# Kernel tuning notes

Measured on AMD Instinct MI355X. Metric: run time of the kernel, lower is better.

Reference implementation:

```python
import jax, jax.numpy as jnp
import numpy as np

MAX_THRESHOLD = 0.25  # init kwarg
B, S, D, E = 8, 4096, 512, 8


def setup_inputs() -> dict:
    key = jax.random.key(0)
    ks = jax.random.split(key, 5)
    scale = 1.0 / np.sqrt(D)
    return {
        "inputs": jax.random.normal(ks[0], (B, S, D), dtype=jnp.float32),
        "W_gate": jax.random.normal(ks[1], (D, E), dtype=jnp.float32) * scale,
        "b_gate": jnp.zeros((E,), dtype=jnp.float32),
        "W_thr": jax.random.normal(ks[2], (D, 1), dtype=jnp.float32) * scale,
        "b_thr": jnp.zeros((1,), dtype=jnp.float32),
        "W_exp": jax.random.normal(ks[3], (E, D, D), dtype=jnp.float32) * scale,
        "b_exp": jnp.zeros((E, D), dtype=jnp.float32),
    }


def reference(inputs, W_gate, b_gate, W_thr, b_thr, W_exp, b_exp):
    d = inputs.shape[-1]
    x = inputs.reshape(-1, d)  # [T, D]
    # gating
    gate_logits = jax.nn.softmax(x @ W_gate + b_gate, axis=-1)          # [T, E]
    thresholds = jax.nn.sigmoid(x @ W_thr + b_thr) * MAX_THRESHOLD      # [T, 1]
    adapted = gate_logits - thresholds                                  # [T, E]
    selected = (adapted >= 0).astype(x.dtype)                           # [T, E]
    weights = adapted * selected                                        # [T, E]
    wsum = jnp.sum(weights, axis=-1, keepdims=True)
    wsum = jnp.where(wsum == 0, jnp.ones_like(wsum), wsum)
    weights = weights / wsum
    # dense-equivalent of gather->expert->scatter (weights are 0 where unselected)
    ex_out = jnp.einsum('td,edf->etf', x, W_exp) + b_exp[:, None, :]    # [E, T, D]
    results = jnp.einsum('etf,te->tf', ex_out, weights)                 # [T, D]
    return results.reshape(inputs.shape[:-1] + (results.shape[-1],))
```

## Files before the change

kernel.cpp:

```cpp
#include <hip/hip_runtime.h>


#define T_TOKENS 32768
#define DDIM 512
#define KDIM 4096

typedef __attribute__((ext_vector_type(8))) short short8;
typedef __attribute__((ext_vector_type(4))) float floatx4;
typedef __bf16 bf16x2 __attribute__((ext_vector_type(2)));

__device__ __forceinline__ unsigned short f2bf(float f) {
    unsigned int u = __float_as_uint(f);
    u += 0x7FFFu + ((u >> 16) & 1u);
    return (unsigned short)(u >> 16);
}

__device__ __forceinline__ unsigned int pk2(float a, float b) {
#if __has_builtin(__builtin_amdgcn_cvt_pk_bf16_f32)
    bf16x2 v = __builtin_amdgcn_cvt_pk_bf16_f32(a, b);
    return __builtin_bit_cast(unsigned int, v);
#else
    return (unsigned int)f2bf(a) | ((unsigned int)f2bf(b) << 16);
#endif
}

__device__ __forceinline__ void async_copy16(const void* g, void* l) {
    __builtin_amdgcn_global_load_lds(
        (const __attribute__((address_space(1))) void*)g,
        (__attribute__((address_space(3))) void*)l, 16, 0, 0);
}

__global__ __launch_bounds__(256) void gating_cvt(
    const float* __restrict__ x, const float* __restrict__ Wg,
    const float* __restrict__ bg, const float* __restrict__ Wt,
    const float* __restrict__ bt, float* __restrict__ wbuf,
    unsigned short* __restrict__ Xbf)
{
    __shared__ float sW[512 * 12];
    const int tid = threadIdx.x;
    for (int i = tid; i < 512 * 9; i += 256) {
        int d = i / 9, e = i - d * 9;
        sW[d * 12 + e] = (e < 8) ? Wg[d * 8 + e] : Wt[d];
    }
    __syncthreads();

    const int t = blockIdx.x * 64 + (tid >> 2);
    const int q = tid & 3;
    float g[9];
#pragma unroll
    for (int e = 0; e < 9; ++e) g[e] = 0.f;

    const float4* xr = (const float4*)(x + (size_t)t * 512 + q * 128);
    for (int i = 0; i < 32; ++i) {
        float4 v = xr[i];
        float xv[4] = {v.x, v.y, v.z, v.w};
        const float* wp = &sW[(q * 128 + i * 4) * 12];
#pragma unroll
        for (int c = 0; c < 4; ++c) {
            const float* w = wp + c * 12;
#pragma unroll
            for (int e = 0; e < 9; ++e) g[e] = fmaf(xv[c], w[e], g[e]);
        }
    }
#pragma unroll
    for (int e = 0; e < 9; ++e) {
        g[e] += __shfl_xor(g[e], 1);
        g[e] += __shfl_xor(g[e], 2);
    }
    if (q == 0) {
#pragma unroll
        for (int e = 0; e < 8; ++e) g[e] += bg[e];
        g[8] += bt[0];
        float m = g[0];
#pragma unroll
        for (int e = 1; e < 8; ++e) m = fmaxf(m, g[e]);
        float s = 0.f;
        float p[8];
#pragma unroll
        for (int e = 0; e < 8; ++e) { p[e] = __expf(g[e] - m); s += p[e]; }
        const float inv = 1.f / s;
        const float thr = 0.25f / (1.f + __expf(-g[8]));
        float w8[8];
        float ws = 0.f;
#pragma unroll
        for (int e = 0; e < 8; ++e) {
            float a = p[e] * inv - thr;
            w8[e] = a > 0.f ? a : 0.f;
            ws += w8[e];
        }
        if (ws == 0.f) ws = 1.f;
        const float invw = 1.f / ws;
        float4 o0, o1;
        o0.x = w8[0] * invw; o0.y = w8[1] * invw; o0.z = w8[2] * invw; o0.w = w8[3] * invw;
        o1.x = w8[4] * invw; o1.y = w8[5] * invw; o1.z = w8[6] * invw; o1.w = w8[7] * invw;
        float4* op = (float4*)(wbuf + (size_t)t * 8);
        op[0] = o0;
        op[1] = o1;
    }

    const size_t base = (size_t)blockIdx.x * 64 * 512;
    const float4* xs = (const float4*)(x + base);
    uint2* xd = (uint2*)(Xbf + base);
#pragma unroll 4
    for (int it = 0; it < 32; ++it) {
        float4 v = xs[it * 256 + tid];
        uint2 pk;
        pk.x = pk2(v.x, v.y);
        pk.y = pk2(v.z, v.w);
        xd[it * 256 + tid] = pk;
    }
}

__global__ __launch_bounds__(256) void build_bt(
    const float* __restrict__ Wexp, unsigned short* __restrict__ Bt)
{
    __shared__ float tile[64][65];
    const int k0 = blockIdx.x * 64;
    const int n0 = blockIdx.y * 64;
    const int tid = threadIdx.x;
    const int r = tid >> 4, cq = tid & 15;
#pragma unroll
    for (int p = 0; p < 4; ++p) {
        const int rr = p * 16 + r;
        const float4 v = *(const float4*)(Wexp + (size_t)(k0 + rr) * 512 + n0 + cq * 4);
        tile[rr][cq * 4 + 0] = v.x;
        tile[rr][cq * 4 + 1] = v.y;
        tile[rr][cq * 4 + 2] = v.z;
        tile[rr][cq * 4 + 3] = v.w;
    }
    __syncthreads();
    const int rn = tid >> 2;
    const int kq = tid & 3;
    alignas(16) unsigned short buf[16];
#pragma unroll
    for (int j = 0; j < 16; ++j) buf[j] = f2bf(tile[kq * 16 + j][rn]);
    unsigned short* dst = Bt + (size_t)(n0 + rn) * KDIM + k0 + kq * 16;
    *(uint4*)(dst) = *(const uint4*)(buf);
    *(uint4*)(dst + 8) = *(const uint4*)(buf + 8);
}

__global__ __launch_bounds__(256, 2) void moe_gemm(
    const unsigned short* __restrict__ Xbf, const float* __restrict__ wbuf,
    const float* __restrict__ bexp, const unsigned short* __restrict__ Bt,
    float* __restrict__ out)
{
    __shared__ alignas(16) unsigned short As[2 * 128 * 64];
    __shared__ alignas(16) unsigned short Bs[2 * 128 * 64];
    __shared__ float sWbT[8 * 128];
    __shared__ float sBb[8 * 128];

    const int tid = threadIdx.x;
    const int wave = tid >> 6;
    const int lane = tid & 63;
    const int wm = wave >> 1;
    const int wn = wave & 1;
    const int lm = lane & 15;
    const int lq = lane >> 4;
    const int brow = lane >> 3;
    const int cg = (lane & 7) ^ brow;

    const int lin = blockIdx.x;
    const int g = lin & 7;
    const int j_ = lin >> 3;
    const int t0 = (g * 32 + (j_ >> 2)) * 128;
    const int n0 = (j_ & 3) * 128;

    {
        const int row = tid >> 1, half = tid & 1;
        const float4 wv4 = *(const float4*)(wbuf + (size_t)(t0 + row) * 8 + half * 4);
        sWbT[(half * 4 + 0) * 128 + row] = wv4.x;
        sWbT[(half * 4 + 1) * 128 + row] = wv4.y;
        sWbT[(half * 4 + 2) * 128 + row] = wv4.z;
        sWbT[(half * 4 + 3) * 128 + row] = wv4.w;
    }
    ((float4*)sBb)[tid] = *(const float4*)(bexp + (size_t)(tid >> 5) * 512 + n0 + (tid & 31) * 4);

#define STAGE_A(d0, buf)                                                        \
    {                                                                           \
        _Pragma("unroll")                                                       \
        for (int i = 0; i < 4; ++i)                                             \
            async_copy16(Xbf + (size_t)(t0 + wave * 32 + i * 8 + brow) * 512 + (d0) + cg * 8, \
                         As + (buf) * 8192 + (wave * 32 + i * 8) * 64);         \
    }

#define STAGE_B(k0, buf)                                                        \
    {                                                                           \
        _Pragma("unroll")                                                       \
        for (int i = 0; i < 4; ++i)                                             \
            async_copy16(Bt + (size_t)(n0 + wave * 32 + i * 8 + brow) * KDIM + (k0) + cg * 8, \
                         Bs + (buf) * 8192 + (wave * 32 + i * 8) * 64);         \
    }

    STAGE_A(0, 0);
    STAGE_B(0, 0);
    __syncthreads();

    floatx4 acc[4][4], tmp[4][4];
#pragma unroll
    for (int i = 0; i < 4; ++i)
#pragma unroll
        for (int j = 0; j < 4; ++j) acc[i][j] = (floatx4){0.f, 0.f, 0.f, 0.f};

#pragma unroll
    for (int j = 0; j < 4; ++j) {
        const float bb = sBb[0 * 128 + wn * 64 + j * 16 + lm];
#pragma unroll
        for (int i = 0; i < 4; ++i) tmp[i][j] = (floatx4){bb, bb, bb, bb};
    }

#pragma unroll 2
    for (int s = 0; s < 64; ++s) {
        const int nb = s & 1;
        if (s < 63) {
            STAGE_A((((s + 1) & 7) << 6), nb ^ 1);
            STAGE_B(((s + 1) << 6), nb ^ 1);
        }
        const unsigned short* Ab = As + nb * 8192;
        const unsigned short* Bb = Bs + nb * 8192;
#pragma unroll
        for (int kk = 0; kk < 2; ++kk) {
            const int ch = kk * 4 + lq;
            short8 a[4], b[4];
#pragma unroll
            for (int i = 0; i < 4; ++i) {
                const int row = wm * 64 + i * 16 + lm;
                a[i] = *(const short8*)(Ab + row * 64 + ((ch ^ (row & 7)) << 3));
            }
#pragma unroll
            for (int j = 0; j < 4; ++j) {
                const int row = wn * 64 + j * 16 + lm;
                b[j] = *(const short8*)(Bb + row * 64 + ((ch ^ (row & 7)) << 3));
            }
#pragma unroll
            for (int i = 0; i < 4; ++i)
#pragma unroll
                for (int j = 0; j < 4; ++j)
                    tmp[i][j] = __builtin_amdgcn_mfma_f32_16x16x32_bf16(
                        a[i], b[j], tmp[i][j], 0, 0, 0);
        }
        if ((s & 7) == 7) {
            const int e = s >> 3;
#pragma unroll
            for (int i = 0; i < 4; ++i) {
                const float4 wq = *(const float4*)(sWbT + e * 128 + wm * 64 + i * 16 + lq * 4);
#pragma unroll
                for (int j = 0; j < 4; ++j) {
                    acc[i][j][0] = fmaf(wq.x, tmp[i][j][0], acc[i][j][0]);
                    acc[i][j][1] = fmaf(wq.y, tmp[i][j][1], acc[i][j][1]);
                    acc[i][j][2] = fmaf(wq.z, tmp[i][j][2], acc[i][j][2]);
                    acc[i][j][3] = fmaf(wq.w, tmp[i][j][3], acc[i][j][3]);
                }
            }
            if (s < 63) {
#pragma unroll
                for (int j = 0; j < 4; ++j) {
                    const float bb = sBb[(e + 1) * 128 + wn * 64 + j * 16 + lm];
#pragma unroll
                    for (int i = 0; i < 4; ++i) tmp[i][j] = (floatx4){bb, bb, bb, bb};
                }
            }
        }
        __syncthreads();
    }

#pragma unroll
    for (int i = 0; i < 4; ++i)
#pragma unroll
        for (int r = 0; r < 4; ++r) {
            const int rowl = wm * 64 + i * 16 + lq * 4 + r;
            float* op = out + (size_t)(t0 + rowl) * 512 + n0 + wn * 64 + lm;
#pragma unroll
            for (int j = 0; j < 4; ++j) op[j * 16] = acc[i][j][r];
        }
#undef STAGE_A
#undef STAGE_B
}

extern "C" void kernel_launch(void* const* d_in, const int* in_sizes, int n_in,
                              void* d_out, int out_size, void* d_ws, size_t ws_size,
                              hipStream_t stream) {
    const float* x   = (const float*)d_in[0];
    const float* Wg  = (const float*)d_in[1];
    const float* bg  = (const float*)d_in[2];
    const float* Wt  = (const float*)d_in[3];
    const float* bt  = (const float*)d_in[4];
    const float* Wex = (const float*)d_in[5];
    const float* bex = (const float*)d_in[6];
    float* out = (float*)d_out;

    unsigned short* Xbf = (unsigned short*)d_ws;
    unsigned short* Bt  = (unsigned short*)((char*)d_ws + (size_t)T_TOKENS * DDIM * 2);
    float* wbuf = (float*)((char*)d_ws + (size_t)T_TOKENS * DDIM * 2
                                       + (size_t)DDIM * KDIM * 2);

    gating_cvt<<<T_TOKENS / 64, 256, 0, stream>>>(x, Wg, bg, Wt, bt, wbuf, Xbf);
    build_bt<<<dim3(KDIM / 64, DDIM / 64), 256, 0, stream>>>(Wex, Bt);
    moe_gemm<<<1024, 256, 0, stream>>>(Xbf, wbuf, bex, Bt, out);
}
```

Measured before the change: 287.3 us.

## Enlarge GEMM tile to 128x256 with triple-buffered pipeline and epilogue bias

The MoE GEMM now uses 512-thread blocks with 128x256 output tiles (8 waves in a 2x4 grid), halving the grid and reusing each A tile across twice as many columns. Shared-memory staging moves from double to triple buffering, with prefetch two stages ahead. Each step now waits on partial vmcnt and a raw s_barrier instead of a full __syncthreads, and MFMA sections get raised wave priority. The expert bias is moved out of the per-expert accumulator init into a single weighted sum in the epilogue, which removes the sBb shared buffer. Risks include lower occupancy from the larger LDS footprint (about 147KB) and register pressure with 512 threads at launch bound 2.

After: 322.1 us. +12.1%, slower.

```diff
diff --git a/kernel.cpp b/kernel.cpp
--- a/kernel.cpp
+++ b/kernel.cpp
@@ -4,6 +4,8 @@
 #define T_TOKENS 32768
 #define DDIM 512
 #define KDIM 4096
+#define SLOTA 8192
+#define SLOTB 16384
 
 typedef __attribute__((ext_vector_type(8))) short short8;
 typedef __attribute__((ext_vector_type(4))) float floatx4;
@@ -139,21 +141,20 @@
     *(uint4*)(dst + 8) = *(const uint4*)(buf + 8);
 }
 
-__global__ __launch_bounds__(256, 2) void moe_gemm(
+__global__ __launch_bounds__(512, 2) void moe_gemm(
     const unsigned short* __restrict__ Xbf, const float* __restrict__ wbuf,
     const float* __restrict__ bexp, const unsigned short* __restrict__ Bt,
     float* __restrict__ out)
 {
-    __shared__ alignas(16) unsigned short As[2 * 128 * 64];
-    __shared__ alignas(16) unsigned short Bs[2 * 128 * 64];
+    __shared__ alignas(16) unsigned short As[3 * 128 * 64];
+    __shared__ alignas(16) unsigned short Bs[3 * 256 * 64];
     __shared__ float sWbT[8 * 128];
-    __shared__ float sBb[8 * 128];
 
     const int tid = threadIdx.x;
     const int wave = tid >> 6;
     const int lane = tid & 63;
-    const int wm = wave >> 1;
-    const int wn = wave & 1;
+    const int wm = wave >> 2;
+    const int wn = wave & 3;
     const int lm = lane & 15;
     const int lq = lane >> 4;
     const int brow = lane >> 3;
@@ -162,61 +163,52 @@
     const int lin = blockIdx.x;
     const int g = lin & 7;
     const int j_ = lin >> 3;
-    const int t0 = (g * 32 + (j_ >> 2)) * 128;
-    const int n0 = (j_ & 3) * 128;
+    const int t0 = (g * 32 + (j_ >> 1)) * 128;
+    const int n0 = (j_ & 1) * 256;
 
     {
-        const int row = tid >> 1, half = tid & 1;
-        const float4 wv4 = *(const float4*)(wbuf + (size_t)(t0 + row) * 8 + half * 4);
-        sWbT[(half * 4 + 0) * 128 + row] = wv4.x;
-        sWbT[(half * 4 + 1) * 128 + row] = wv4.y;
-        sWbT[(half * 4 + 2) * 128 + row] = wv4.z;
-        sWbT[(half * 4 + 3) * 128 + row] = wv4.w;
-    }
-    ((float4*)sBb)[tid] = *(const float4*)(bexp + (size_t)(tid >> 5) * 512 + n0 + (tid & 31) * 4);
-
-#define STAGE_A(d0, buf)                                                        \
+        const int row = tid & 127, q = tid >> 7;
+        const float2 w2 = *(const float2*)(wbuf + (size_t)(t0 + row) * 8 + q * 2);
+        sWbT[(q * 2 + 0) * 128 + row] = w2.x;
+        sWbT[(q * 2 + 1) * 128 + row] = w2.y;
+    }
+
+#define STAGE(s_, slot_)                                                        \
     {                                                                           \
+        const int d0_ = ((s_) & 7) << 6;                                        \
+        _Pragma("unroll")                                                       \
+        for (int i = 0; i < 2; ++i)                                             \
+            async_copy16(Xbf + (size_t)(t0 + wave * 16 + i * 8 + brow) * 512 + d0_ + cg * 8, \
+                         As + (slot_) * SLOTA + (wave * 16 + i * 8) * 64);      \
+        const int k0_ = (s_) << 6;                                              \
         _Pragma("unroll")                                                       \
         for (int i = 0; i < 4; ++i)                                             \
-            async_copy16(Xbf + (size_t)(t0 + wave * 32 + i * 8 + brow) * 512 + (d0) + cg * 8, \
-                         As + (buf) * 8192 + (wave * 32 + i * 8) * 64);         \
-    }
-
-#define STAGE_B(k0, buf)                                                        \
-    {                                                                           \
-        _Pragma("unroll")                                                       \
-        for (int i = 0; i < 4; ++i)                                             \
-            async_copy16(Bt + (size_t)(n0 + wave * 32 + i * 8 + brow) * KDIM + (k0) + cg * 8, \
-                         Bs + (buf) * 8192 + (wave * 32 + i * 8) * 64);         \
-    }
-
-    STAGE_A(0, 0);
-    STAGE_B(0, 0);
+            async_copy16(Bt + (size_t)(n0 + wave * 32 + i * 8 + brow) * KDIM + k0_ + cg * 8, \
+                         Bs + (slot_) * SLOTB + (wave * 32 + i * 8) * 64);      \
+    }
+
+    STAGE(0, 0);
+    STAGE(1, 1);
     __syncthreads();
 
     floatx4 acc[4][4], tmp[4][4];
 #pragma unroll
     for (int i = 0; i < 4; ++i)
 #pragma unroll
-        for (int j = 0; j < 4; ++j) acc[i][j] = (floatx4){0.f, 0.f, 0.f, 0.f};
-
-#pragma unroll
-    for (int j = 0; j < 4; ++j) {
-        const float bb = sBb[0 * 128 + wn * 64 + j * 16 + lm];
-#pragma unroll
-        for (int i = 0; i < 4; ++i) tmp[i][j] = (floatx4){bb, bb, bb, bb};
-    }
-
-#pragma unroll 2
+        for (int j = 0; j < 4; ++j) {
+            acc[i][j] = (floatx4){0.f, 0.f, 0.f, 0.f};
+            tmp[i][j] = (floatx4){0.f, 0.f, 0.f, 0.f};
+        }
+
+    int sl = 0;
     for (int s = 0; s < 64; ++s) {
-        const int nb = s & 1;
-        if (s < 63) {
-            STAGE_A((((s + 1) & 7) << 6), nb ^ 1);
-            STAGE_B(((s + 1) << 6), nb ^ 1);
-        }
-        const unsigned short* Ab = As + nb * 8192;
-        const unsigned short* Bb = Bs + nb * 8192;
+        if (s < 62) {
+            const int sl2 = (sl >= 1) ? sl - 1 : 2;
+            STAGE(s + 2, sl2);
+        }
+        const unsigned short* Ab = As + sl * SLOTA;
+        const unsigned short* Bb = Bs + sl * SLOTB;
+        __builtin_amdgcn_s_setprio(1);
 #pragma unroll
         for (int kk = 0; kk < 2; ++kk) {
             const int ch = kk * 4 + lq;
@@ -238,6 +230,7 @@
                     tmp[i][j] = __builtin_amdgcn_mfma_f32_16x16x32_bf16(
                         a[i], b[j], tmp[i][j], 0, 0, 0);
         }
+        __builtin_amdgcn_s_setprio(0);
         if ((s & 7) == 7) {
             const int e = s >> 3;
 #pragma unroll
@@ -249,31 +242,48 @@
                     acc[i][j][1] = fmaf(wq.y, tmp[i][j][1], acc[i][j][1]);
                     acc[i][j][2] = fmaf(wq.z, tmp[i][j][2], acc[i][j][2]);
                     acc[i][j][3] = fmaf(wq.w, tmp[i][j][3], acc[i][j][3]);
+                    tmp[i][j] = (floatx4){0.f, 0.f, 0.f, 0.f};
                 }
             }
-            if (s < 63) {
-#pragma unroll
-                for (int j = 0; j < 4; ++j) {
-                    const float bb = sBb[(e + 1) * 128 + wn * 64 + j * 16 + lm];
-#pragma unroll
-                    for (int i = 0; i < 4; ++i) tmp[i][j] = (floatx4){bb, bb, bb, bb};
-                }
-            }
-        }
-        __syncthreads();
-    }
-
+        }
+        if (s < 62) {
+            asm volatile("s_waitcnt vmcnt(6)" ::: "memory");
+        } else if (s == 62) {
+            asm volatile("s_waitcnt vmcnt(0)" ::: "memory");
+        }
+        if (s < 63) __builtin_amdgcn_s_barrier();
+        sl = (sl >= 2) ? 0 : sl + 1;
+    }
+
+    float bc[4][8];
+#pragma unroll
+    for (int j = 0; j < 4; ++j) {
+        const int col = n0 + wn * 64 + j * 16 + lm;
+#pragma unroll
+        for (int e = 0; e < 8; ++e) bc[j][e] = bexp[e * 512 + col];
+    }
 #pragma unroll
     for (int i = 0; i < 4; ++i)
 #pragma unroll
         for (int r = 0; r < 4; ++r) {
             const int rowl = wm * 64 + i * 16 + lq * 4 + r;
+            const float4 w0 = *(const float4*)(wbuf + (size_t)(t0 + rowl) * 8);
+            const float4 w1 = *(const float4*)(wbuf + (size_t)(t0 + rowl) * 8 + 4);
             float* op = out + (size_t)(t0 + rowl) * 512 + n0 + wn * 64 + lm;
 #pragma unroll
-            for (int j = 0; j < 4; ++j) op[j * 16] = acc[i][j][r];
-        }
-#undef STAGE_A
-#undef STAGE_B
+            for (int j = 0; j < 4; ++j) {
+                float bias = w0.x * bc[j][0];
+                bias = fmaf(w0.y, bc[j][1], bias);
+                bias = fmaf(w0.z, bc[j][2], bias);
+                bias = fmaf(w0.w, bc[j][3], bias);
+                bias = fmaf(w1.x, bc[j][4], bias);
+                bias = fmaf(w1.y, bc[j][5], bias);
+                bias = fmaf(w1.z, bc[j][6], bias);
+                bias = fmaf(w1.w, bc[j][7], bias);
+                op[j * 16] = acc[i][j][r] + bias;
+            }
+        }
+#undef STAGE
 }
 
 extern "C" void kernel_launch(void* const* d_in, const int* in_sizes, int n_in,
@@ -295,5 +305,5 @@
 
     gating_cvt<<<T_TOKENS / 64, 256, 0, stream>>>(x, Wg, bg, Wt, bt, wbuf, Xbf);
     build_bt<<<dim3(KDIM / 64, DDIM / 64), 256, 0, stream>>>(Wex, Bt);
-    moe_gemm<<<1024, 256, 0, stream>>>(Xbf, wbuf, bex, Bt, out);
-}
+    moe_gemm<<<512, 512, 0, stream>>>(Xbf, wbuf, bex, Bt, out);
+}
```

## Load A fragments directly to registers and triple-buffer B in LDS

Applied to the files above, without the earlier changes.

Removes the LDS staging for the activation tile: each wave loads its A fragments straight from global memory into registers, double-buffered across steps. B moves to a three-slot LDS ring with a manual vmcnt wait plus barrier, and s_setprio is raised around the MFMA blocks. The per-expert bias seeding of the accumulator is replaced by a weighted bias sum added at the epilogue. This halves LDS traffic and deepens the prefetch, at the cost of more registers and uncoalesced direct global loads for A.

After: 441.8 us. 53.8% more time.

```diff
diff --git a/kernel.cpp b/kernel.cpp
--- a/kernel.cpp
+++ b/kernel.cpp
@@ -4,6 +4,7 @@
 #define T_TOKENS 32768
 #define DDIM 512
 #define KDIM 4096
+#define SLOTB 8192
 
 typedef __attribute__((ext_vector_type(8))) short short8;
 typedef __attribute__((ext_vector_type(4))) float floatx4;
@@ -144,10 +145,8 @@
     const float* __restrict__ bexp, const unsigned short* __restrict__ Bt,
     float* __restrict__ out)
 {
-    __shared__ alignas(16) unsigned short As[2 * 128 * 64];
-    __shared__ alignas(16) unsigned short Bs[2 * 128 * 64];
+    __shared__ alignas(16) unsigned short Bs[3 * SLOTB];
     __shared__ float sWbT[8 * 128];
-    __shared__ float sBb[8 * 128];
 
     const int tid = threadIdx.x;
     const int wave = tid >> 6;
@@ -173,107 +172,154 @@
         sWbT[(half * 4 + 2) * 128 + row] = wv4.z;
         sWbT[(half * 4 + 3) * 128 + row] = wv4.w;
     }
-    ((float4*)sBb)[tid] = *(const float4*)(bexp + (size_t)(tid >> 5) * 512 + n0 + (tid & 31) * 4);
-
-#define STAGE_A(d0, buf)                                                        \
-    {                                                                           \
+
+    const unsigned short* xbase = Xbf + (size_t)(t0 + wm * 64 + lm) * 512 + lq * 8;
+
+#define STAGE_B(s_, slot_)                                                      \
+    {                                                                           \
+        const int k0_ = (s_) << 6;                                              \
         _Pragma("unroll")                                                       \
         for (int i = 0; i < 4; ++i)                                             \
-            async_copy16(Xbf + (size_t)(t0 + wave * 32 + i * 8 + brow) * 512 + (d0) + cg * 8, \
-                         As + (buf) * 8192 + (wave * 32 + i * 8) * 64);         \
-    }
-
-#define STAGE_B(k0, buf)                                                        \
-    {                                                                           \
+            async_copy16(Bt + (size_t)(n0 + wave * 32 + i * 8 + brow) * KDIM + k0_ + cg * 8, \
+                         Bs + (slot_) * SLOTB + (wave * 32 + i * 8) * 64);      \
+    }
+
+#define LOAD_A(s_, dst)                                                         \
+    {                                                                           \
+        const int d0_ = ((s_) & 7) << 6;                                        \
         _Pragma("unroll")                                                       \
         for (int i = 0; i < 4; ++i)                                             \
-            async_copy16(Bt + (size_t)(n0 + wave * 32 + i * 8 + brow) * KDIM + (k0) + cg * 8, \
-                         Bs + (buf) * 8192 + (wave * 32 + i * 8) * 64);         \
-    }
-
-    STAGE_A(0, 0);
+            _Pragma("unroll")                                                   \
+            for (int kk = 0; kk < 2; ++kk)                                      \
+                dst[i][kk] = *(const short8*)(xbase + i * 16 * 512 + d0_ + kk * 32); \
+    }
+
+#define COMPUTE(slot_, areg)                                                    \
+    {                                                                           \
+        const unsigned short* Bb = Bs + (slot_) * SLOTB;                        \
+        __builtin_amdgcn_s_setprio(1);                                          \
+        _Pragma("unroll")                                                       \
+        for (int kk = 0; kk < 2; ++kk) {                                        \
+            const int ch = kk * 4 + lq;                                         \
+            short8 b[4];                                                        \
+            _Pragma("unroll")                                                   \
+            for (int j = 0; j < 4; ++j) {                                       \
+                const int row = wn * 64 + j * 16 + lm;                          \
+                b[j] = *(const short8*)(Bb + row * 64 + ((ch ^ (row & 7)) << 3)); \
+            }                                                                   \
+            _Pragma("unroll")                                                   \
+            for (int i = 0; i < 4; ++i)                                         \
+                _Pragma("unroll")                                               \
+                for (int j = 0; j < 4; ++j)                                     \
+                    tmp[i][j] = __builtin_amdgcn_mfma_f32_16x16x32_bf16(        \
+                        areg[i][kk], b[j], tmp[i][j], 0, 0, 0);                 \
+        }                                                                       \
+        __builtin_amdgcn_s_setprio(0);                                          \
+    }
+
+#define FOLD(e_)                                                                \
+    {                                                                           \
+        _Pragma("unroll")                                                       \
+        for (int i = 0; i < 4; ++i) {                                           \
+            const float4 wq = *(const float4*)(sWbT + (e_) * 128 + wm * 64 + i * 16 + lq * 4); \
+            _Pragma("unroll")                                                   \
+            for (int j = 0; j < 4; ++j) {                                       \
+                acc[i][j][0] = fmaf(wq.x, tmp[i][j][0], acc[i][j][0]);          \
+                acc[i][j][1] = fmaf(wq.y, tmp[i][j][1], acc[i][j][1]);          \
+                acc[i][j][2] = fmaf(wq.z, tmp[i][j][2], acc[i][j][2]);          \
+                acc[i][j][3] = fmaf(wq.w, tmp[i][j][3], acc[i][j][3]);          \
+                tmp[i][j] = (floatx4){0.f, 0.f, 0.f, 0.f};                      \
+            }                                                                   \
+        }                                                                       \
+    }
+
+#define SYNC12()                                                                \
+    {                                                                           \
+        __builtin_amdgcn_sched_barrier(0);                                      \
+        asm volatile("s_waitcnt vmcnt(12)" ::: "memory");                       \
+        __builtin_amdgcn_s_barrier();                                           \
+        __builtin_amdgcn_sched_barrier(0);                                      \
+    }
+
+    floatx4 acc[4][4], tmp[4][4];
+#pragma unroll
+    for (int i = 0; i < 4; ++i)
+#pragma unroll
+        for (int j = 0; j < 4; ++j) {
+            acc[i][j] = (floatx4){0.f, 0.f, 0.f, 0.f};
+            tmp[i][j] = (floatx4){0.f, 0.f, 0.f, 0.f};
+        }
+
+    short8 a0[4][2], a1[4][2];
+
     STAGE_B(0, 0);
+    STAGE_B(1, 1);
+    LOAD_A(0, a0);
     __syncthreads();
 
-    floatx4 acc[4][4], tmp[4][4];
-#pragma unroll
-    for (int i = 0; i < 4; ++i)
-#pragma unroll
-        for (int j = 0; j < 4; ++j) acc[i][j] = (floatx4){0.f, 0.f, 0.f, 0.f};
-
+    int sl = 0;
+    for (int m = 0; m < 32; ++m) {
+        const int s0 = 2 * m;
+        const int sl1 = (sl >= 2) ? sl - 2 : sl + 1;
+        const int sl2 = (sl >= 1) ? sl - 1 : sl + 2;
+
+        if (m < 31) STAGE_B(s0 + 2, sl2);
+        LOAD_A(s0 + 1, a1);
+        COMPUTE(sl, a0);
+        if (m < 31) {
+            SYNC12();
+        } else {
+            __builtin_amdgcn_sched_barrier(0);
+            asm volatile("s_waitcnt vmcnt(8)" ::: "memory");
+            __builtin_amdgcn_s_barrier();
+            __builtin_amdgcn_sched_barrier(0);
+        }
+
+        const int s1 = s0 + 1;
+        if (m < 31) {
+            STAGE_B(s1 + 2, sl);
+            LOAD_A(s1 + 1, a0);
+        }
+        COMPUTE(sl1, a1);
+        if ((m & 3) == 3) FOLD(s1 >> 3);
+        if (m < 31) SYNC12();
+
+        sl = sl2;
+    }
+
+    float bc[4][8];
 #pragma unroll
     for (int j = 0; j < 4; ++j) {
-        const float bb = sBb[0 * 128 + wn * 64 + j * 16 + lm];
-#pragma unroll
-        for (int i = 0; i < 4; ++i) tmp[i][j] = (floatx4){bb, bb, bb, bb};
-    }
-
-#pragma unroll 2
-    for (int s = 0; s < 64; ++s) {
-        const int nb = s & 1;
-        if (s < 63) {
-            STAGE_A((((s + 1) & 7) << 6), nb ^ 1);
-            STAGE_B(((s + 1) << 6), nb ^ 1);
-        }
-        const unsigned short* Ab = As + nb * 8192;
-        const unsigned short* Bb = Bs + nb * 8192;
-#pragma unroll
-        for (int kk = 0; kk < 2; ++kk) {
-            const int ch = kk * 4 + lq;
-            short8 a[4], b[4];
-#pragma unroll
-            for (int i = 0; i < 4; ++i) {
-                const int row = wm * 64 + i * 16 + lm;
-                a[i] = *(const short8*)(Ab + row * 64 + ((ch ^ (row & 7)) << 3));
-            }
-#pragma unroll
-            for (int j = 0; j < 4; ++j) {
-                const int row = wn * 64 + j * 16 + lm;
-                b[j] = *(const short8*)(Bb + row * 64 + ((ch ^ (row & 7)) << 3));
-            }
-#pragma unroll
-            for (int i = 0; i < 4; ++i)
-#pragma unroll
-                for (int j = 0; j < 4; ++j)
-                    tmp[i][j] = __builtin_amdgcn_mfma_f32_16x16x32_bf16(
-                        a[i], b[j], tmp[i][j], 0, 0, 0);
-        }
-        if ((s & 7) == 7) {
-            const int e = s >> 3;
-#pragma unroll
-            for (int i = 0; i < 4; ++i) {
-                const float4 wq = *(const float4*)(sWbT + e * 128 + wm * 64 + i * 16 + lq * 4);
-#pragma unroll
-                for (int j = 0; j < 4; ++j) {
-                    acc[i][j][0] = fmaf(wq.x, tmp[i][j][0], acc[i][j][0]);
-                    acc[i][j][1] = fmaf(wq.y, tmp[i][j][1], acc[i][j][1]);
-                    acc[i][j][2] = fmaf(wq.z, tmp[i][j][2], acc[i][j][2]);
-                    acc[i][j][3] = fmaf(wq.w, tmp[i][j][3], acc[i][j][3]);
-                }
-            }
-            if (s < 63) {
-#pragma unroll
-                for (int j = 0; j < 4; ++j) {
-                    const float bb = sBb[(e + 1) * 128 + wn * 64 + j * 16 + lm];
-#pragma unroll
-                    for (int i = 0; i < 4; ++i) tmp[i][j] = (floatx4){bb, bb, bb, bb};
-                }
-            }
-        }
-        __syncthreads();
-    }
-
+        const int col = n0 + wn * 64 + j * 16 + lm;
+#pragma unroll
+        for (int e = 0; e < 8; ++e) bc[j][e] = bexp[e * 512 + col];
+    }
 #pragma unroll
     for (int i = 0; i < 4; ++i)
 #pragma unroll
         for (int r = 0; r < 4; ++r) {
             const int rowl = wm * 64 + i * 16 + lq * 4 + r;
+            const float4 w0 = *(const float4*)(wbuf + (size_t)(t0 + rowl) * 8);
+            const float4 w1 = *(const float4*)(wbuf + (size_t)(t0 + rowl) * 8 + 4);
             float* op = out + (size_t)(t0 + rowl) * 512 + n0 + wn * 64 + lm;
 #pragma unroll
-            for (int j = 0; j < 4; ++j) op[j * 16] = acc[i][j][r];
-        }
-#undef STAGE_A
+            for (int j = 0; j < 4; ++j) {
+                float bias = w0.x * bc[j][0];
+                bias = fmaf(w0.y, bc[j][1], bias);
+                bias = fmaf(w0.z, bc[j][2], bias);
+                bias = fmaf(w0.w, bc[j][3], bias);
+                bias = fmaf(w1.x, bc[j][4], bias);
+                bias = fmaf(w1.y, bc[j][5], bias);
+                bias = fmaf(w1.z, bc[j][6], bias);
+                bias = fmaf(w1.w, bc[j][7], bias);
+                op[j * 16] = acc[i][j][r] + bias;
+            }
+        }
 #undef STAGE_B
+#undef LOAD_A
+#undef COMPUTE
+#undef FOLD
+#undef SYNC12
 }
 
 extern "C" void kernel_launch(void* const* d_in, const int* in_sizes, int n_in,
```

## Sort tokens by expert mask and skip unselected experts per tile

Applied to the files above, without the earlier changes.

Gating now emits a per-token expert bitmask and a histogram. A scan and scatter pass then builds a permutation that groups tokens with identical masks, plus a per-tile OR of masks. The GEMM gathers permuted token rows, iterates only over experts present in its tile, and scatters outputs back. Gating, X conversion and weight transposition are merged into one launch. This adds several small launches and atomics, and the work saved depends on how homogeneous the masks are within a tile.

New measurement: 302.3 us. 5.2% more time.

```diff
diff --git a/kernel.cpp b/kernel.cpp
--- a/kernel.cpp
+++ b/kernel.cpp
@@ -30,124 +30,191 @@
         (__attribute__((address_space(3))) void*)l, 16, 0, 0);
 }
 
-__global__ __launch_bounds__(256) void gating_cvt(
+__global__ __launch_bounds__(256) void zero_ctrl(int* __restrict__ ctrl) {
+    const int tid = threadIdx.x;
+#pragma unroll
+    for (int i = 0; i < 3; ++i) ctrl[i * 256 + tid] = 0;
+}
+
+__global__ __launch_bounds__(256) void gating_cvt_bt(
     const float* __restrict__ x, const float* __restrict__ Wg,
     const float* __restrict__ bg, const float* __restrict__ Wt,
     const float* __restrict__ bt, float* __restrict__ wbuf,
-    unsigned short* __restrict__ Xbf)
+    unsigned short* __restrict__ Xbf,
+    const float* __restrict__ Wexp, unsigned short* __restrict__ Bt,
+    int* __restrict__ tmask, int* __restrict__ hist)
 {
-    __shared__ float sW[512 * 12];
     const int tid = threadIdx.x;
-    for (int i = tid; i < 512 * 9; i += 256) {
-        int d = i / 9, e = i - d * 9;
-        sW[d * 12 + e] = (e < 8) ? Wg[d * 8 + e] : Wt[d];
-    }
+
+    if (blockIdx.x >= 512) {
+        __shared__ float tile[64][65];
+        const int bb = blockIdx.x - 512;
+        const int k0 = (bb & 63) * 64;
+        const int n0 = (bb >> 6) * 64;
+        const int r = tid >> 4, cq = tid & 15;
+#pragma unroll
+        for (int p = 0; p < 4; ++p) {
+            const int rr = p * 16 + r;
+            const float4 v = *(const float4*)(Wexp + (size_t)(k0 + rr) * 512 + n0 + cq * 4);
+            tile[rr][cq * 4 + 0] = v.x;
+            tile[rr][cq * 4 + 1] = v.y;
+            tile[rr][cq * 4 + 2] = v.z;
+            tile[rr][cq * 4 + 3] = v.w;
+        }
+        __syncthreads();
+        const int rn = tid >> 2;
+        const int kq = tid & 3;
+        alignas(16) unsigned short buf[16];
+#pragma unroll
+        for (int j = 0; j < 16; ++j) buf[j] = f2bf(tile[kq * 16 + j][rn]);
+        unsigned short* dst = Bt + (size_t)(n0 + rn) * KDIM + k0 + kq * 16;
+        *(uint4*)(dst) = *(const uint4*)(buf);
+        *(uint4*)(dst + 8) = *(const uint4*)(buf + 8);
+        return;
+    }
+
+    __shared__ int shist[256];
+    shist[tid] = 0;
     __syncthreads();
 
-    const int t = blockIdx.x * 64 + (tid >> 2);
-    const int q = tid & 3;
-    float g[9];
-#pragma unroll
-    for (int e = 0; e < 9; ++e) g[e] = 0.f;
-
-    const float4* xr = (const float4*)(x + (size_t)t * 512 + q * 128);
-    for (int i = 0; i < 32; ++i) {
-        float4 v = xr[i];
-        float xv[4] = {v.x, v.y, v.z, v.w};
-        const float* wp = &sW[(q * 128 + i * 4) * 12];
-#pragma unroll
-        for (int c = 0; c < 4; ++c) {
-            const float* w = wp + c * 12;
-#pragma unroll
-            for (int e = 0; e < 9; ++e) g[e] = fmaf(xv[c], w[e], g[e]);
-        }
-    }
-#pragma unroll
-    for (int e = 0; e < 9; ++e) {
-        g[e] += __shfl_xor(g[e], 1);
-        g[e] += __shfl_xor(g[e], 2);
-    }
-    if (q == 0) {
-#pragma unroll
-        for (int e = 0; e < 8; ++e) g[e] += bg[e];
-        g[8] += bt[0];
-        float m = g[0];
-#pragma unroll
-        for (int e = 1; e < 8; ++e) m = fmaxf(m, g[e]);
-        float s = 0.f;
-        float p[8];
-#pragma unroll
-        for (int e = 0; e < 8; ++e) { p[e] = __expf(g[e] - m); s += p[e]; }
-        const float inv = 1.f / s;
-        const float thr = 0.25f / (1.f + __expf(-g[8]));
-        float w8[8];
-        float ws = 0.f;
-#pragma unroll
-        for (int e = 0; e < 8; ++e) {
-            float a = p[e] * inv - thr;
-            w8[e] = a > 0.f ? a : 0.f;
-            ws += w8[e];
-        }
-        if (ws == 0.f) ws = 1.f;
-        const float invw = 1.f / ws;
-        float4 o0, o1;
-        o0.x = w8[0] * invw; o0.y = w8[1] * invw; o0.z = w8[2] * invw; o0.w = w8[3] * invw;
-        o1.x = w8[4] * invw; o1.y = w8[5] * invw; o1.z = w8[6] * invw; o1.w = w8[7] * invw;
-        float4* op = (float4*)(wbuf + (size_t)t * 8);
-        op[0] = o0;
-        op[1] = o1;
-    }
-
-    const size_t base = (size_t)blockIdx.x * 64 * 512;
-    const float4* xs = (const float4*)(x + base);
-    uint2* xd = (uint2*)(Xbf + base);
-#pragma unroll 4
-    for (int it = 0; it < 32; ++it) {
-        float4 v = xs[it * 256 + tid];
-        uint2 pk;
-        pk.x = pk2(v.x, v.y);
-        pk.y = pk2(v.z, v.w);
-        xd[it * 256 + tid] = pk;
-    }
-}
-
-__global__ __launch_bounds__(256) void build_bt(
-    const float* __restrict__ Wexp, unsigned short* __restrict__ Bt)
+    const int wv = tid >> 6;
+    const int lane = tid & 63;
+
+    float4 wg[16];
+    {
+        const float4* wgp = (const float4*)(Wg + lane * 64);
+#pragma unroll
+        for (int c = 0; c < 16; ++c) wg[c] = wgp[c];
+    }
+    const float4 wt0 = *(const float4*)(Wt + lane * 8);
+    const float4 wt1 = *(const float4*)(Wt + lane * 8 + 4);
+    const float bgv[8] = {bg[0], bg[1], bg[2], bg[3], bg[4], bg[5], bg[6], bg[7]};
+    const float btv = bt[0];
+
+    for (int it = 0; it < 16; ++it) {
+        const int t = blockIdx.x * 64 + wv * 16 + it;
+        const float* xp = x + (size_t)t * 512 + lane * 8;
+        const float4 a0 = *(const float4*)(xp);
+        const float4 a1 = *(const float4*)(xp + 4);
+
+        uint2 pk0, pk1;
+        pk0.x = pk2(a0.x, a0.y);
+        pk0.y = pk2(a0.z, a0.w);
+        pk1.x = pk2(a1.x, a1.y);
+        pk1.y = pk2(a1.z, a1.w);
+        uint2* xd = (uint2*)(Xbf + (size_t)t * 512 + lane * 8);
+        xd[0] = pk0;
+        xd[1] = pk1;
+
+        const float xv[8] = {a0.x, a0.y, a0.z, a0.w, a1.x, a1.y, a1.z, a1.w};
+        const float wtv[8] = {wt0.x, wt0.y, wt0.z, wt0.w, wt1.x, wt1.y, wt1.z, wt1.w};
+        float g[9];
+#pragma unroll
+        for (int e = 0; e < 9; ++e) g[e] = 0.f;
+#pragma unroll
+        for (int j = 0; j < 8; ++j) {
+            const float4 wlo = wg[j * 2];
+            const float4 whi = wg[j * 2 + 1];
+            g[0] = fmaf(xv[j], wlo.x, g[0]);
+            g[1] = fmaf(xv[j], wlo.y, g[1]);
+            g[2] = fmaf(xv[j], wlo.z, g[2]);
+            g[3] = fmaf(xv[j], wlo.w, g[3]);
+            g[4] = fmaf(xv[j], whi.x, g[4]);
+            g[5] = fmaf(xv[j], whi.y, g[5]);
+            g[6] = fmaf(xv[j], whi.z, g[6]);
+            g[7] = fmaf(xv[j], whi.w, g[7]);
+            g[8] = fmaf(xv[j], wtv[j], g[8]);
+        }
+#pragma unroll
+        for (int e = 0; e < 9; ++e) {
+            g[e] += __shfl_xor(g[e], 1);
+            g[e] += __shfl_xor(g[e], 2);
+            g[e] += __shfl_xor(g[e], 4);
+            g[e] += __shfl_xor(g[e], 8);
+            g[e] += __shfl_xor(g[e], 16);
+            g[e] += __shfl_xor(g[e], 32);
+        }
+        if (lane == 0) {
+#pragma unroll
+            for (int e = 0; e < 8; ++e) g[e] += bgv[e];
+            g[8] += btv;
+            float m = g[0];
+#pragma unroll
+            for (int e = 1; e < 8; ++e) m = fmaxf(m, g[e]);
+            float s = 0.f;
+            float p[8];
+#pragma unroll
+            for (int e = 0; e < 8; ++e) { p[e] = __expf(g[e] - m); s += p[e]; }
+            const float inv = 1.f / s;
+            const float thr = 0.25f / (1.f + __expf(-g[8]));
+            float w8[8];
+            float ws = 0.f;
+            int mk = 0;
+#pragma unroll
+            for (int e = 0; e < 8; ++e) {
+                float a = p[e] * inv - thr;
+                w8[e] = a > 0.f ? a : 0.f;
+                if (w8[e] > 0.f) mk |= (1 << e);
+                ws += w8[e];
+            }
+            if (ws == 0.f) ws = 1.f;
+            const float invw = 1.f / ws;
+            float4 o0, o1;
+            o0.x = w8[0] * invw; o0.y = w8[1] * invw; o0.z = w8[2] * invw; o0.w = w8[3] * invw;
+            o1.x = w8[4] * invw; o1.y = w8[5] * invw; o1.z = w8[6] * invw; o1.w = w8[7] * invw;
+            float4* op = (float4*)(wbuf + (size_t)t * 8);
+            op[0] = o0;
+            op[1] = o1;
+            tmask[t] = mk;
+            atomicAdd(&shist[mk], 1);
+        }
+    }
+    __syncthreads();
+    const int v = shist[tid];
+    if (v) atomicAdd(&hist[tid], v);
+}
+
+__global__ __launch_bounds__(256) void scan_offsets(
+    const int* __restrict__ hist, int* __restrict__ offset)
 {
-    __shared__ float tile[64][65];
-    const int k0 = blockIdx.x * 64;
-    const int n0 = blockIdx.y * 64;
+    __shared__ int tmp[256];
     const int tid = threadIdx.x;
-    const int r = tid >> 4, cq = tid & 15;
-#pragma unroll
-    for (int p = 0; p < 4; ++p) {
-        const int rr = p * 16 + r;
-        const float4 v = *(const float4*)(Wexp + (size_t)(k0 + rr) * 512 + n0 + cq * 4);
-        tile[rr][cq * 4 + 0] = v.x;
-        tile[rr][cq * 4 + 1] = v.y;
-        tile[rr][cq * 4 + 2] = v.z;
-        tile[rr][cq * 4 + 3] = v.w;
-    }
+    const int v = hist[tid];
+    tmp[tid] = v;
     __syncthreads();
-    const int rn = tid >> 2;
-    const int kq = tid & 3;
-    alignas(16) unsigned short buf[16];
-#pragma unroll
-    for (int j = 0; j < 16; ++j) buf[j] = f2bf(tile[kq * 16 + j][rn]);
-    unsigned short* dst = Bt + (size_t)(n0 + rn) * KDIM + k0 + kq * 16;
-    *(uint4*)(dst) = *(const uint4*)(buf);
-    *(uint4*)(dst + 8) = *(const uint4*)(buf + 8);
+    int acc = tmp[tid];
+    for (int d = 1; d < 256; d <<= 1) {
+        int t = (tid >= d) ? tmp[tid - d] : 0;
+        __syncthreads();
+        acc += t;
+        tmp[tid] = acc;
+        __syncthreads();
+    }
+    offset[tid] = acc - v;
+}
+
+__global__ __launch_bounds__(256) void scatter_perm(
+    const int* __restrict__ tmask, const int* __restrict__ offset,
+    int* __restrict__ cursor, int* __restrict__ perm, int* __restrict__ tilemask)
+{
+    const int t = blockIdx.x * 256 + threadIdx.x;
+    const int mk = tmask[t];
+    const int pos = offset[mk] + atomicAdd(&cursor[mk], 1);
+    perm[pos] = t;
+    if (mk) atomicOr(&tilemask[pos >> 7], mk);
 }
 
 __global__ __launch_bounds__(256, 2) void moe_gemm(
     const unsigned short* __restrict__ Xbf, const float* __restrict__ wbuf,
     const float* __restrict__ bexp, const unsigned short* __restrict__ Bt,
+    const int* __restrict__ perm, const int* __restrict__ tilemask,
     float* __restrict__ out)
 {
-    __shared__ alignas(16) unsigned short As[2 * 128 * 64];
-    __shared__ alignas(16) unsigned short Bs[2 * 128 * 64];
+    __shared__ alignas(16) unsigned short As[2 * 8192];
+    __shared__ alignas(16) unsigned short Bs[2 * 8192];
     __shared__ float sWbT[8 * 128];
     __shared__ float sBb[8 * 128];
+    __shared__ int sPerm[128];
 
     const int tid = threadIdx.x;
     const int wave = tid >> 6;
@@ -162,12 +229,17 @@
     const int lin = blockIdx.x;
     const int g = lin & 7;
     const int j_ = lin >> 3;
-    const int t0 = (g * 32 + (j_ >> 2)) * 128;
+    const int tt = (j_ >> 2) * 8 + g;
+    const int t0 = tt * 128;
     const int n0 = (j_ & 3) * 128;
+
+    if (tid < 128) sPerm[tid] = perm[t0 + tid];
+    __syncthreads();
 
     {
         const int row = tid >> 1, half = tid & 1;
-        const float4 wv4 = *(const float4*)(wbuf + (size_t)(t0 + row) * 8 + half * 4);
+        const int tok = sPerm[row];
+        const float4 wv4 = *(const float4*)(wbuf + (size_t)tok * 8 + half * 4);
         sWbT[(half * 4 + 0) * 128 + row] = wv4.x;
         sWbT[(half * 4 + 1) * 128 + row] = wv4.y;
         sWbT[(half * 4 + 2) * 128 + row] = wv4.z;
@@ -175,92 +247,112 @@
     }
     ((float4*)sBb)[tid] = *(const float4*)(bexp + (size_t)(tid >> 5) * 512 + n0 + (tid & 31) * 4);
 
-#define STAGE_A(d0, buf)                                                        \
+    int tokA[4];
+#pragma unroll
+    for (int i = 0; i < 4; ++i) tokA[i] = sPerm[wave * 32 + i * 8 + brow];
+
+    const int tm = tilemask[tt];
+
+#define STAGE_A(d0_, buf_)                                                      \
     {                                                                           \
         _Pragma("unroll")                                                       \
         for (int i = 0; i < 4; ++i)                                             \
-            async_copy16(Xbf + (size_t)(t0 + wave * 32 + i * 8 + brow) * 512 + (d0) + cg * 8, \
-                         As + (buf) * 8192 + (wave * 32 + i * 8) * 64);         \
-    }
-
-#define STAGE_B(k0, buf)                                                        \
+            async_copy16(Xbf + (size_t)tokA[i] * 512 + (d0_) + cg * 8,          \
+                         As + (buf_) * 8192 + (wave * 32 + i * 8) * 64);        \
+    }
+#define STAGE_B(k0_, buf_)                                                      \
     {                                                                           \
         _Pragma("unroll")                                                       \
         for (int i = 0; i < 4; ++i)                                             \
-            async_copy16(Bt + (size_t)(n0 + wave * 32 + i * 8 + brow) * KDIM + (k0) + cg * 8, \
-                         Bs + (buf) * 8192 + (wave * 32 + i * 8) * 64);         \
-    }
-
-    STAGE_A(0, 0);
-    STAGE_B(0, 0);
-    __syncthreads();
-
-    floatx4 acc[4][4], tmp[4][4];
+            async_copy16(Bt + (size_t)(n0 + wave * 32 + i * 8 + brow) * KDIM + (k0_) + cg * 8, \
+                         Bs + (buf_) * 8192 + (wave * 32 + i * 8) * 64);        \
+    }
+
+    floatx4 acc[4][4];
 #pragma unroll
     for (int i = 0; i < 4; ++i)
 #pragma unroll
         for (int j = 0; j < 4; ++j) acc[i][j] = (floatx4){0.f, 0.f, 0.f, 0.f};
 
-#pragma unroll
-    for (int j = 0; j < 4; ++j) {
-        const float bb = sBb[0 * 128 + wn * 64 + j * 16 + lm];
-#pragma unroll
-        for (int i = 0; i < 4; ++i) tmp[i][j] = (floatx4){bb, bb, bb, bb};
-    }
-
-#pragma unroll 2
-    for (int s = 0; s < 64; ++s) {
-        const int nb = s & 1;
-        if (s < 63) {
-            STAGE_A((((s + 1) & 7) << 6), nb ^ 1);
-            STAGE_B(((s + 1) << 6), nb ^ 1);
-        }
-        const unsigned short* Ab = As + nb * 8192;
-        const unsigned short* Bb = Bs + nb * 8192;
-#pragma unroll
-        for (int kk = 0; kk < 2; ++kk) {
-            const int ch = kk * 4 + lq;
-            short8 a[4], b[4];
-#pragma unroll
-            for (int i = 0; i < 4; ++i) {
-                const int row = wm * 64 + i * 16 + lm;
-                a[i] = *(const short8*)(Ab + row * 64 + ((ch ^ (row & 7)) << 3));
+    if (tm) {
+        floatx4 tmp[4][4];
+        int m = tm;
+        int ec = __ffs(m) - 1;
+        const int ne = __popc(m);
+
+        STAGE_A(0, 0);
+        STAGE_B(ec * 512, 0);
+        __syncthreads();
+
+#pragma unroll
+        for (int j = 0; j < 4; ++j) {
+            const float bb = sBb[ec * 128 + wn * 64 + j * 16 + lm];
+#pragma unroll
+            for (int i = 0; i < 4; ++i) tmp[i][j] = (floatx4){bb, bb, bb, bb};
+        }
+
+        for (int ei = 0; ei < ne; ++ei) {
+            const int m2 = m & (m - 1);
+            const int en = m2 ? (__ffs(m2) - 1) : 0;
+#pragma unroll
+            for (int ks = 0; ks < 8; ++ks) {
+                const int nb = ks & 1;
+                const bool last = (ei == ne - 1) && (ks == 7);
+                if (!last) {
+                    const int ep = (ks < 7) ? ec : en;
+                    const int d0n = ((ks + 1) & 7) << 6;
+                    STAGE_A(d0n, nb ^ 1);
+                    STAGE_B(ep * 512 + d0n, nb ^ 1);
+                }
+                const unsigned short* Ab = As + nb * 8192;
+                const unsigned short* Bb = Bs + nb * 8192;
+#pragma unroll
+                for (int kk = 0; kk < 2; ++kk) {
+                    const int ch = kk * 4 + lq;
+                    short8 a[4], b[4];
+#pragma unroll
+                    for (int i = 0; i < 4; ++i) {
+                        const int row = wm * 64 + i * 16 + lm;
+                        a[i] = *(const short8*)(Ab + row * 64 + ((ch ^ (row & 7)) << 3));
+                    }
+#pragma unroll
+                    for (int j = 0; j < 4; ++j) {
+                        const int row = wn * 64 + j * 16 + lm;
+                        b[j] = *(const short8*)(Bb + row * 64 + ((ch ^ (row & 7)) << 3));
+                    }
+#pragma unroll
+                    for (int i = 0; i < 4; ++i)
+#pragma unroll
+                        for (int j = 0; j < 4; ++j)
+                            tmp[i][j] = __builtin_amdgcn_mfma_f32_16x16x32_bf16(
+                                a[i], b[j], tmp[i][j], 0, 0, 0);
+                }
+                if (ks == 7) {
+#pragma unroll
+                    for (int i = 0; i < 4; ++i) {
+                        const float4 wq = *(const float4*)(sWbT + ec * 128 + wm * 64 + i * 16 + lq * 4);
+#pragma unroll
+                        for (int j = 0; j < 4; ++j) {
+                            acc[i][j][0] = fmaf(wq.x, tmp[i][j][0], acc[i][j][0]);
+                            acc[i][j][1] = fmaf(wq.y, tmp[i][j][1], acc[i][j][1]);
+                            acc[i][j][2] = fmaf(wq.z, tmp[i][j][2], acc[i][j][2]);
+                            acc[i][j][3] = fmaf(wq.w, tmp[i][j][3], acc[i][j][3]);
+                        }
+                    }
+                    if (ei < ne - 1) {
+#pragma unroll
+                        for (int j = 0; j < 4; ++j) {
+                            const float bb = sBb[en * 128 + wn * 64 + j * 16 + lm];
+#pragma unroll
+                            for (int i = 0; i < 4; ++i) tmp[i][j] = (floatx4){bb, bb, bb, bb};
+                        }
+                    }
+                }
+                __syncthreads();
             }
-#pragma unroll
-            for (int j = 0; j < 4; ++j) {
-                const int row = wn * 64 + j * 16 + lm;
-                b[j] = *(const short8*)(Bb + row * 64 + ((ch ^ (row & 7)) << 3));
-            }
-#pragma unroll
-            for (int i = 0; i < 4; ++i)
-#pragma unroll
-                for (int j = 0; j < 4; ++j)
-                    tmp[i][j] = __builtin_amdgcn_mfma_f32_16x16x32_bf16(
-                        a[i], b[j], tmp[i][j], 0, 0, 0);
-        }
-        if ((s & 7) == 7) {
-            const int e = s >> 3;
-#pragma unroll
-            for (int i = 0; i < 4; ++i) {
-                const float4 wq = *(const float4*)(sWbT + e * 128 + wm * 64 + i * 16 + lq * 4);
-#pragma unroll
-                for (int j = 0; j < 4; ++j) {
-                    acc[i][j][0] = fmaf(wq.x, tmp[i][j][0], acc[i][j][0]);
-                    acc[i][j][1] = fmaf(wq.y, tmp[i][j][1], acc[i][j][1]);
-                    acc[i][j][2] = fmaf(wq.z, tmp[i][j][2], acc[i][j][2]);
-                    acc[i][j][3] = fmaf(wq.w, tmp[i][j][3], acc[i][j][3]);
-                }
-            }
-            if (s < 63) {
-#pragma unroll
-                for (int j = 0; j < 4; ++j) {
-                    const float bb = sBb[(e + 1) * 128 + wn * 64 + j * 16 + lm];
-#pragma unroll
-                    for (int i = 0; i < 4; ++i) tmp[i][j] = (floatx4){bb, bb, bb, bb};
-                }
-            }
-        }
-        __syncthreads();
+            m = m2;
+            ec = en;
+        }
     }
 
 #pragma unroll
@@ -268,7 +360,8 @@
 #pragma unroll
         for (int r = 0; r < 4; ++r) {
             const int rowl = wm * 64 + i * 16 + lq * 4 + r;
-            float* op = out + (size_t)(t0 + rowl) * 512 + n0 + wn * 64 + lm;
+            const int tok = sPerm[rowl];
+            float* op = out + (size_t)tok * 512 + n0 + wn * 64 + lm;
 #pragma unroll
             for (int j = 0; j < 4; ++j) op[j * 16] = acc[i][j][r];
         }
@@ -288,12 +381,22 @@
     const float* bex = (const float*)d_in[6];
     float* out = (float*)d_out;
 
-    unsigned short* Xbf = (unsigned short*)d_ws;
-    unsigned short* Bt  = (unsigned short*)((char*)d_ws + (size_t)T_TOKENS * DDIM * 2);
-    float* wbuf = (float*)((char*)d_ws + (size_t)T_TOKENS * DDIM * 2
-                                       + (size_t)DDIM * KDIM * 2);
-
-    gating_cvt<<<T_TOKENS / 64, 256, 0, stream>>>(x, Wg, bg, Wt, bt, wbuf, Xbf);
-    build_bt<<<dim3(KDIM / 64, DDIM / 64), 256, 0, stream>>>(Wex, Bt);
-    moe_gemm<<<1024, 256, 0, stream>>>(Xbf, wbuf, bex, Bt, out);
-}
+    char* p = (char*)d_ws;
+    unsigned short* Xbf = (unsigned short*)p;           p += (size_t)T_TOKENS * DDIM * 2;
+    unsigned short* Bt  = (unsigned short*)p;           p += (size_t)DDIM * KDIM * 2;
+    float* wbuf = (float*)p;                            p += (size_t)T_TOKENS * 8 * 4;
+    int* tmask = (int*)p;                               p += (size_t)T_TOKENS * 4;
+    int* perm = (int*)p;                                p += (size_t)T_TOKENS * 4;
+    int* ctrl = (int*)p;
+    int* hist = ctrl;
+    int* cursor = ctrl + 256;
+    int* tilemask = ctrl + 512;
+    int* offset = ctrl + 768;
+
+    zero_ctrl<<<1, 256, 0, stream>>>(ctrl);
+    gating_cvt_bt<<<1024, 256, 0, stream>>>(x, Wg, bg, Wt, bt, wbuf, Xbf, Wex, Bt,
+                                            tmask, hist);
+    scan_offsets<<<1, 256, 0, stream>>>(hist, offset);
+    scatter_perm<<<T_TOKENS / 256, 256, 0, stream>>>(tmask, offset, cursor, perm, tilemask);
+    moe_gemm<<<1024, 256, 0, stream>>>(Xbf, wbuf, bex, Bt, perm, tilemask, out);
+}
```
